# Kernel tuning notes

Measured on AMD Instinct MI355X. Metric: run time of the kernel, lower is better.

The kernel has to match this reference:

```python
import jax, jax.numpy as jnp
import numpy as np


def _lstm_step(x, h, c, Wih, Whh, bih, bhh):
    # PyTorch LSTMCell gate order: i, f, g, o
    g = x @ Wih.T + bih + h @ Whh.T + bhh
    i, f, gg, o = jnp.split(g, 4, axis=1)
    c = jax.nn.sigmoid(f) * c + jax.nn.sigmoid(i) * jnp.tanh(gg)
    h = jax.nn.sigmoid(o) * jnp.tanh(c)
    return h, c


def _canvas2seq(canvas):
    # Valid objects (row-sum >= 0) compacted to the front, rest padded with -1.
    mask = canvas.sum(axis=2) >= 0                       # [B, 25]
    order = jnp.argsort(jnp.where(mask, 0, 1), axis=1, stable=True)
    gathered = jnp.take_along_axis(canvas, order[:, :, None], axis=1)
    smask = jnp.take_along_axis(mask, order, axis=1)
    return jnp.where(smask[:, :, None], gathered, jnp.float32(-1.0))


def _canvas_encode(canvas, Wobj, bobj, ce_Wih, ce_Whh, ce_bih, ce_bhh):
    seq = _canvas2seq(canvas)                            # [B, 25, 4]
    x = seq @ Wobj.T + bobj                              # [B, 25, 64]
    B = x.shape[0]
    h = jnp.zeros((B, 64), x.dtype)
    c = jnp.zeros((B, 64), x.dtype)

    def step(carry, xt):
        h, c = carry
        h, c = _lstm_step(xt, h, c, ce_Wih, ce_Whh, ce_bih, ce_bhh)
        return (h, c), None

    (h, _), _ = jax.lax.scan(step, (h, c), jnp.swapaxes(x, 0, 1))
    return h


def setup_inputs() -> dict:
    key = jax.random.key(0)
    ks = jax.random.split(key, 16)
    B, T, V = 256, 65, 10000
    IN, H = 64, 128
    s = 0.05
    inp = {}
    inp["inst"] = jax.random.randint(ks[0], (B, T), 0, V)
    inp["prev_canvas"] = jax.random.uniform(ks[1], (B, 25, 4), dtype=jnp.float32)
    inp["final_canvas"] = jax.random.uniform(ks[2], (B, 25, 4), dtype=jnp.float32)
    inp["target_obj"] = jax.random.normal(ks[3], (B, 4), dtype=jnp.float32)
    inp["embed_W"] = jax.random.normal(ks[4], (V + 1, IN), dtype=jnp.float32) * s
    inp["Wih"] = jax.random.normal(ks[5], (4 * H, IN), dtype=jnp.float32) * s
    inp["Whh"] = jax.random.normal(ks[6], (4 * H, H), dtype=jnp.float32) * s
    inp["bih"] = jnp.zeros((4 * H,), jnp.float32)
    inp["bhh"] = jnp.zeros((4 * H,), jnp.float32)
    inp["Wout"] = jax.random.normal(ks[7], (V + 1, H), dtype=jnp.float32) * s
    inp["bout"] = jnp.zeros((V + 1,), jnp.float32)
    inp["Wtgt"] = jax.random.normal(ks[8], (IN, 4), dtype=jnp.float32) * s
    inp["btgt"] = jnp.zeros((IN,), jnp.float32)
    inp["Wobj"] = jax.random.normal(ks[9], (64, 4), dtype=jnp.float32) * s
    inp["bobj"] = jnp.zeros((64,), jnp.float32)
    inp["ce_Wih"] = jax.random.normal(ks[10], (256, 64), dtype=jnp.float32) * s
    inp["ce_Whh"] = jax.random.normal(ks[11], (256, 64), dtype=jnp.float32) * s
    inp["ce_bih"] = jnp.zeros((256,), jnp.float32)
    inp["ce_bhh"] = jnp.zeros((256,), jnp.float32)
    return inp


def reference(inst, prev_canvas, final_canvas, target_obj,
              embed_W, Wih, Whh, bih, bhh, Wout, bout,
              Wtgt, btgt, Wobj, bobj, ce_Wih, ce_Whh, ce_bih, ce_bhh):
    B, H = inst.shape[0], 128
    tgt_emb = target_obj @ Wtgt.T + btgt                 # [B, 64]
    enc = (_canvas_encode(prev_canvas, Wobj, bobj, ce_Wih, ce_Whh, ce_bih, ce_bhh)
           + _canvas_encode(final_canvas, Wobj, bobj, ce_Wih, ce_Whh, ce_bih, ce_bhh))
    h = jnp.zeros((B, H), jnp.float32)
    c = jnp.zeros((B, H), jnp.float32)
    h, c = _lstm_step(enc, h, c, Wih, Whh, bih, bhh)
    h, c = _lstm_step(tgt_emb, h, c, Wih, Whh, bih, bhh)

    tokens = inst[:, :-1].T                              # [T-1, B]

    def step(carry, it):
        h, c = carry
        xt = embed_W[it]                                 # [B, 64]
        h, c = _lstm_step(xt, h, c, Wih, Whh, bih, bhh)
        lp = jax.nn.log_softmax(h @ Wout.T + bout, axis=1)
        return (h, c), lp

    _, lps = jax.lax.scan(step, (h, c), tokens)          # [T-1, B, V+1]
    return jnp.swapaxes(lps, 0, 1)                       # [B, T-1, V+1]
```

## Files before the change

kernel.cpp:

```cpp
#include <hip/hip_runtime.h>
#include <stdint.h>

typedef __attribute__((ext_vector_type(4))) float f32x4;
typedef __attribute__((ext_vector_type(8))) short s16x8;
typedef __attribute__((ext_vector_type(8))) unsigned short us8;

__device__ __forceinline__ float bf2f(unsigned short u){
  union { unsigned int i; float f; } v; v.i = ((unsigned int)u) << 16; return v.f;
}
__device__ __forceinline__ unsigned short f2bf(float f){
  union { float f; unsigned int i; } v; v.f = f;
  unsigned int r = v.i + 0x7FFFu + ((v.i >> 16) & 1u);
  return (unsigned short)(r >> 16);
}
__device__ __forceinline__ float sigm(float x){ return 1.0f / (1.0f + __expf(-x)); }

#define NA (10240*128)
#define NB 10240
#define ND 512
#define NE (256*64)
#define NF 32768

__global__ void k_prep(const float* __restrict__ Wout, const float* __restrict__ bout,
                       const float* __restrict__ bih,  const float* __restrict__ bhh,
                       const float* __restrict__ tobj, const float* __restrict__ Wtgt,
                       const float* __restrict__ btgt,
                       const float* __restrict__ ceWih, const float* __restrict__ ceWhh,
                       unsigned short* __restrict__ WoutP, float* __restrict__ boutP,
                       float* __restrict__ bsum, float* __restrict__ tgt,
                       unsigned short* __restrict__ cePack)
{
  int tid = blockIdx.x * 256 + threadIdx.x;
  if (tid < NA){
    int vv = tid >> 7, k = tid & 127;
    float val = (vv < 10001) ? Wout[vv*128 + k] : 0.0f;
    WoutP[tid] = f2bf(val);
  } else if (tid < NA+NB){
    int vv = tid - NA;
    boutP[vv] = (vv < 10001) ? bout[vv] : -1e30f;
  } else if (tid < NA+NB+ND){
    int g = tid - NA - NB;
    bsum[g] = bih[g] + bhh[g];
  } else if (tid < NA+NB+ND+NE){
    int i = tid - NA - NB - ND; int b = i >> 6, j = i & 63;
    const float* to = tobj + b*4; const float* wt = Wtgt + j*4;
    tgt[i] = btgt[j] + to[0]*wt[0] + to[1]*wt[1] + to[2]*wt[2] + to[3]*wt[3];
  } else if (tid < NA+NB+ND+NE+NF){
    int i = tid - NA - NB - ND - NE;
    int half = i >> 14;
    int r = (i >> 6) & 255;
    int k = i & 63;
    int k8 = k >> 3;
    int slot = ((k8 ^ (r & 7)) << 3) | (k & 7);
    const float* src = half ? ceWhh : ceWih;
    cePack[half*16384 + r*64 + slot] = f2bf(src[r*64 + k]);
  }
}

__global__ __launch_bounds__(256) void k_canvas(
    const float* __restrict__ prevC, const float* __restrict__ finC,
    const float* __restrict__ Wobj,  const float* __restrict__ bobj,
    const unsigned short* __restrict__ cePack,
    const float* __restrict__ cebih, const float* __restrict__ cebhh,
    float* __restrict__ encP, float* __restrict__ encF)
{
  __shared__ unsigned short wih[256*64] __attribute__((aligned(16)));
  __shared__ unsigned short whh[256*64] __attribute__((aligned(16)));
  __shared__ float seq[25*4];
  __shared__ float xb[64] __attribute__((aligned(16)));
  __shared__ float hb[2][64] __attribute__((aligned(16)));
  __shared__ float gates[256];
  __shared__ float wobj_s[256];
  __shared__ float bobj_s[64];
  __shared__ float bsum_ce[256];

  int tid = threadIdx.x;
  int b = blockIdx.x & 255;
  int which = blockIdx.x >> 8;
  const float* canvas = (which ? finC : prevC) + b*100;

  {
    const us8* cp = (const us8*)cePack;
    us8* wl = (us8*)wih;
    us8* hl = (us8*)whh;
    for (int i = tid; i < 2048; i += 256){
      wl[i] = cp[i];
      hl[i] = cp[2048 + i];
    }
  }
  wobj_s[tid] = Wobj[tid];
  if (tid < 64) bobj_s[tid] = bobj[tid];
  bsum_ce[tid] = cebih[tid] + cebhh[tid];
  if (tid < 64) hb[0][tid] = 0.0f;
  if (tid == 0){
    int pos = 0;
    for (int i = 0; i < 25; i++){
      float a0=canvas[i*4+0], a1=canvas[i*4+1], a2=canvas[i*4+2], a3=canvas[i*4+3];
      if (a0+a1+a2+a3 >= 0.0f){
        seq[pos*4+0]=a0; seq[pos*4+1]=a1; seq[pos*4+2]=a2; seq[pos*4+3]=a3; pos++;
      }
    }
    for (; pos < 25; pos++){
      seq[pos*4+0]=-1.0f; seq[pos*4+1]=-1.0f; seq[pos*4+2]=-1.0f; seq[pos*4+3]=-1.0f;
    }
  }
  __syncthreads();

  float creg = 0.0f;
  int cur = 0;
  const float4* x4 = (const float4*)xb;

  for (int t = 0; t < 25; t++){
    if (tid < 64){
      float a = bobj_s[tid];
      a += wobj_s[tid*4+0]*seq[t*4+0] + wobj_s[tid*4+1]*seq[t*4+1]
         + wobj_s[tid*4+2]*seq[t*4+2] + wobj_s[tid*4+3]*seq[t*4+3];
      xb[tid] = a;
    }
    __syncthreads();
    float acc = bsum_ce[tid];
    const float4* h4 = (const float4*)hb[cur];
    int rowoff = tid*64;
    int sw = tid & 7;
    #pragma unroll
    for (int k8 = 0; k8 < 8; k8++){
      int slot = ((k8 ^ sw) * 8);
      us8 w1 = *reinterpret_cast<const us8*>(&wih[rowoff + slot]);
      us8 w2 = *reinterpret_cast<const us8*>(&whh[rowoff + slot]);
      float4 xa = x4[2*k8], xc = x4[2*k8+1];
      float4 ha = h4[2*k8], hc = h4[2*k8+1];
      acc += bf2f(w1[0])*xa.x + bf2f(w1[1])*xa.y + bf2f(w1[2])*xa.z + bf2f(w1[3])*xa.w;
      acc += bf2f(w1[4])*xc.x + bf2f(w1[5])*xc.y + bf2f(w1[6])*xc.z + bf2f(w1[7])*xc.w;
      acc += bf2f(w2[0])*ha.x + bf2f(w2[1])*ha.y + bf2f(w2[2])*ha.z + bf2f(w2[3])*ha.w;
      acc += bf2f(w2[4])*hc.x + bf2f(w2[5])*hc.y + bf2f(w2[6])*hc.z + bf2f(w2[7])*hc.w;
    }
    gates[tid] = acc;
    __syncthreads();
    if (tid < 64){
      float i_ = sigm(gates[tid]);
      float f_ = sigm(gates[64+tid]);
      float g_ = tanhf(gates[128+tid]);
      float o_ = sigm(gates[192+tid]);
      creg = f_*creg + i_*g_;
      hb[cur^1][tid] = o_ * tanhf(creg);
    }
    __syncthreads();
    cur ^= 1;
  }
  if (tid < 64){
    (which ? encF : encP)[b*64 + tid] = hb[cur][tid];
  }
}

__global__ __launch_bounds__(512, 2) void k_rec(
    const float* __restrict__ Whh, const float* __restrict__ Wih,
    const float* __restrict__ bsum, const int* __restrict__ inst,
    const float* __restrict__ embW, const float* __restrict__ tgt,
    const float* __restrict__ encP, const float* __restrict__ encF,
    unsigned short* __restrict__ Hout)
{
  int b = blockIdx.x;
  int g = threadIdx.x;
  __shared__ float xb[2][64] __attribute__((aligned(16)));
  __shared__ float hb[2][128] __attribute__((aligned(16)));
  __shared__ float gates[512];

  float wreg[128];
  float ureg[64];
  {
    const float4* wrow = (const float4*)(Whh + g*128);
    #pragma unroll
    for (int k4 = 0; k4 < 32; k4++){
      float4 w = wrow[k4];
      wreg[4*k4+0]=w.x; wreg[4*k4+1]=w.y; wreg[4*k4+2]=w.z; wreg[4*k4+3]=w.w;
    }
    const float4* urow = (const float4*)(Wih + g*64);
    #pragma unroll
    for (int k4 = 0; k4 < 16; k4++){
      float4 w = urow[k4];
      ureg[4*k4+0]=w.x; ureg[4*k4+1]=w.y; ureg[4*k4+2]=w.z; ureg[4*k4+3]=w.w;
    }
  }
  float bz = bsum[g];
  float creg = 0.0f;
  if (g < 128) hb[0][g] = 0.0f;
  if (g < 64)  xb[0][g] = encP[b*64+g] + encF[b*64+g];
  int cur = 0;
  __syncthreads();

  for (int s = 0; s < 66; s++){
    float a0 = bz, a1 = 0.0f, a2 = 0.0f, a3 = 0.0f;
    const float4* h4 = (const float4*)hb[cur];
    const float4* x4 = (const float4*)xb[cur];
    #pragma unroll
    for (int k4 = 0; k4 < 32; k4 += 4){
      float4 h0 = h4[k4], h1 = h4[k4+1], h2 = h4[k4+2], h3 = h4[k4+3];
      a0 += wreg[4*k4+0]*h0.x + wreg[4*k4+1]*h0.y + wreg[4*k4+2]*h0.z + wreg[4*k4+3]*h0.w;
      a1 += wreg[4*k4+4]*h1.x + wreg[4*k4+5]*h1.y + wreg[4*k4+6]*h1.z + wreg[4*k4+7]*h1.w;
      a2 += wreg[4*k4+8]*h2.x + wreg[4*k4+9]*h2.y + wreg[4*k4+10]*h2.z + wreg[4*k4+11]*h2.w;
      a3 += wreg[4*k4+12]*h3.x + wreg[4*k4+13]*h3.y + wreg[4*k4+14]*h3.z + wreg[4*k4+15]*h3.w;
    }
    #pragma unroll
    for (int k4 = 0; k4 < 16; k4 += 4){
      float4 x0 = x4[k4], x1 = x4[k4+1], x2 = x4[k4+2], x3 = x4[k4+3];
      a0 += ureg[4*k4+0]*x0.x + ureg[4*k4+1]*x0.y + ureg[4*k4+2]*x0.z + ureg[4*k4+3]*x0.w;
      a1 += ureg[4*k4+4]*x1.x + ureg[4*k4+5]*x1.y + ureg[4*k4+6]*x1.z + ureg[4*k4+7]*x1.w;
      a2 += ureg[4*k4+8]*x2.x + ureg[4*k4+9]*x2.y + ureg[4*k4+10]*x2.z + ureg[4*k4+11]*x2.w;
      a3 += ureg[4*k4+12]*x3.x + ureg[4*k4+13]*x3.y + ureg[4*k4+14]*x3.z + ureg[4*k4+15]*x3.w;
    }
    gates[g] = (a0 + a1) + (a2 + a3);
    __syncthreads();
    if (g < 128){
      float i_ = sigm(gates[g]);
      float f_ = sigm(gates[128+g]);
      float g_ = tanhf(gates[256+g]);
      float o_ = sigm(gates[384+g]);
      creg = f_*creg + i_*g_;
      float h = o_ * tanhf(creg);
      hb[cur^1][g] = h;
      if (s >= 2) Hout[((size_t)(b*64 + (s-2)))*128 + g] = f2bf(h);
    } else if (g < 192 && s < 65){
      int l = g - 128;
      float v;
      if (s + 1 == 1) v = tgt[b*64 + l];
      else { int tok = inst[b*65 + (s - 1)]; v = embW[tok*64 + l]; }
      xb[cur^1][l] = v;
    }
    __syncthreads();
    cur ^= 1;
  }
}

__global__ __launch_bounds__(512, 2) void k_out(
    const unsigned short* __restrict__ Hout, const unsigned short* __restrict__ WoutP,
    const float* __restrict__ boutP, float* __restrict__ out)
{
  extern __shared__ float stage[];
  __shared__ float rs_l[8][64];
  __shared__ float lse_l[64];

  int blk = blockIdx.x;
  int r0 = blk * 64;
  int tid = threadIdx.x;
  int w = tid >> 6;
  int l = tid & 63;
  int lm = l & 15;
  int lq = l >> 4;
  int kof = lq * 8;
  size_t obase = (size_t)r0 * 10001u;

  s16x8 af[4][4];
  #pragma unroll
  for (int c = 0; c < 4; c++){
    const s16x8* ap = (const s16x8*)(Hout + (size_t)(r0 + c*16 + lm)*128 + kof);
    #pragma unroll
    for (int kk = 0; kk < 4; kk++) af[c][kk] = ap[kk*4];
  }

  s16x8 b0[4], b1[4], b2[4];
#define LOADB(dst, tl) { \
    const s16x8* bp_ = (const s16x8*)(WoutP + (size_t)((tl)*16 + lm)*128 + kof); \
    dst[0] = bp_[0]; dst[1] = bp_[4]; dst[2] = bp_[8]; dst[3] = bp_[12]; }

  float rs[4][4] = {};
#define P1C(buf, tl) { \
    f32x4 a0_ = {0,0,0,0}, a1_ = {0,0,0,0}, a2_ = {0,0,0,0}, a3_ = {0,0,0,0}; \
    _Pragma("unroll") \
    for (int kk = 0; kk < 4; kk++){ \
      a0_ = __builtin_amdgcn_mfma_f32_16x16x32_bf16(af[0][kk], buf[kk], a0_, 0, 0, 0); \
      a1_ = __builtin_amdgcn_mfma_f32_16x16x32_bf16(af[1][kk], buf[kk], a1_, 0, 0, 0); \
      a2_ = __builtin_amdgcn_mfma_f32_16x16x32_bf16(af[2][kk], buf[kk], a2_, 0, 0, 0); \
      a3_ = __builtin_amdgcn_mfma_f32_16x16x32_bf16(af[3][kk], buf[kk], a3_, 0, 0, 0); } \
    float bo_ = boutP[(tl)*16 + lm]; \
    _Pragma("unroll") \
    for (int i = 0; i < 4; i++){ \
      rs[0][i] += __expf(a0_[i] + bo_); rs[1][i] += __expf(a1_[i] + bo_); \
      rs[2][i] += __expf(a2_[i] + bo_); rs[3][i] += __expf(a3_[i] + bo_); } }

  {
    int tl = w;
    LOADB(b0, tl); LOADB(b1, tl + 8);
    for (int p = 0; p < 26; p++){
      LOADB(b2, tl + 16); P1C(b0, tl);
      LOADB(b0, tl + 24); P1C(b1, tl + 8);
      LOADB(b1, tl + 32); P1C(b2, tl + 16);
      tl += 24;
    }
    P1C(b0, tl);
    P1C(b1, tl + 8);
  }

  #pragma unroll
  for (int c = 0; c < 4; c++){
    #pragma unroll
    for (int i = 0; i < 4; i++){
      float s = rs[c][i];
      s += __shfl_xor(s, 1); s += __shfl_xor(s, 2);
      s += __shfl_xor(s, 4); s += __shfl_xor(s, 8);
      rs[c][i] = s;
    }
  }
  if (lm == 0){
    #pragma unroll
    for (int c = 0; c < 4; c++)
      #pragma unroll
      for (int i = 0; i < 4; i++)
        rs_l[w][c*16 + lq*4 + i] = rs[c][i];
  }

#define T2(c,q) ((c)*32 + w*4 + (q))
  LOADB(b0, T2(0,0)); LOADB(b1, T2(0,1));

#define BAR() { asm volatile("s_waitcnt lgkmcnt(0)" ::: "memory"); __builtin_amdgcn_s_barrier(); }

  BAR();
  if (tid < 64){
    float s = rs_l[0][tid] + rs_l[1][tid] + rs_l[2][tid] + rs_l[3][tid]
            + rs_l[4][tid] + rs_l[5][tid] + rs_l[6][tid] + rs_l[7][tid];
    lse_l[tid] = logf(s);
  }
  BAR();
  float ml[4][4];
  #pragma unroll
  for (int c = 0; c < 4; c++)
    #pragma unroll
    for (int i = 0; i < 4; i++)
      ml[c][i] = lse_l[c*16 + lq*4 + i];

#define P2C(buf, tl, q) { \
    f32x4 a0_ = {0,0,0,0}, a1_ = {0,0,0,0}, a2_ = {0,0,0,0}, a3_ = {0,0,0,0}; \
    _Pragma("unroll") \
    for (int kk = 0; kk < 4; kk++){ \
      a0_ = __builtin_amdgcn_mfma_f32_16x16x32_bf16(af[0][kk], buf[kk], a0_, 0, 0, 0); \
      a1_ = __builtin_amdgcn_mfma_f32_16x16x32_bf16(af[1][kk], buf[kk], a1_, 0, 0, 0); \
      a2_ = __builtin_amdgcn_mfma_f32_16x16x32_bf16(af[2][kk], buf[kk], a2_, 0, 0, 0); \
      a3_ = __builtin_amdgcn_mfma_f32_16x16x32_bf16(af[3][kk], buf[kk], a3_, 0, 0, 0); } \
    float bo_ = boutP[(tl)*16 + lm]; \
    int colq_ = (w*4 + (q))*16 + lm; \
    _Pragma("unroll") \
    for (int i = 0; i < 4; i++){ \
      stage[(0*16 + lq*4 + i)*520 + colq_] = a0_[i] + bo_ - ml[0][i]; \
      stage[(1*16 + lq*4 + i)*520 + colq_] = a1_[i] + bo_ - ml[1][i]; \
      stage[(2*16 + lq*4 + i)*520 + colq_] = a2_[i] + bo_ - ml[2][i]; \
      stage[(3*16 + lq*4 + i)*520 + colq_] = a3_[i] + bo_ - ml[3][i]; } }

#define WPHASE(c) { \
    int vbase_ = (c)*512; \
    if ((c) < 19){ \
      _Pragma("unroll 4") \
      for (int j = 0; j < 64; j++){ \
        __builtin_nontemporal_store(stage[j*520 + tid], \
            &out[obase + (size_t)j*10001u + (unsigned)(vbase_ + tid)]); } \
    } else { \
      if (tid < 273){ \
        _Pragma("unroll 4") \
        for (int j = 0; j < 64; j++){ \
          __builtin_nontemporal_store(stage[j*520 + tid], \
              &out[obase + (size_t)j*10001u + (unsigned)(vbase_ + tid)]); } } } }

#define CHUNK(ba,bb,bc,c) { \
    LOADB(bc, T2(c,2));   P2C(ba, T2(c,0), 0); \
    LOADB(ba, T2(c,3));   P2C(bb, T2(c,1), 1); \
    LOADB(bb, T2((c)+1,0)); P2C(bc, T2(c,2), 2); \
    LOADB(bc, T2((c)+1,1)); P2C(ba, T2(c,3), 3); \
    BAR(); WPHASE(c); BAR(); }

  for (int cb = 0; cb < 18; cb += 3){
    CHUNK(b0, b1, b2, cb);
    CHUNK(b1, b2, b0, cb + 1);
    CHUNK(b2, b0, b1, cb + 2);
  }
  CHUNK(b0, b1, b2, 18);
  LOADB(b0, T2(19,2)); P2C(b1, T2(19,0), 0);
  LOADB(b1, T2(19,3)); P2C(b2, T2(19,1), 1);
  P2C(b0, T2(19,2), 2);
  P2C(b1, T2(19,3), 3);
  BAR();
  WPHASE(19);
}

extern "C" void kernel_launch(void* const* d_in, const int* in_sizes, int n_in,
                              void* d_out, int out_size, void* d_ws, size_t ws_size,
                              hipStream_t stream)
{
  (void)in_sizes; (void)n_in; (void)out_size; (void)ws_size;
  const int*   inst    = (const int*)  d_in[0];
  const float* prevC   = (const float*)d_in[1];
  const float* finC    = (const float*)d_in[2];
  const float* tobj    = (const float*)d_in[3];
  const float* embW    = (const float*)d_in[4];
  const float* Wih     = (const float*)d_in[5];
  const float* Whh     = (const float*)d_in[6];
  const float* bih     = (const float*)d_in[7];
  const float* bhh     = (const float*)d_in[8];
  const float* Wout    = (const float*)d_in[9];
  const float* bout    = (const float*)d_in[10];
  const float* Wtgt    = (const float*)d_in[11];
  const float* btgt    = (const float*)d_in[12];
  const float* Wobj    = (const float*)d_in[13];
  const float* bobj    = (const float*)d_in[14];
  const float* ceWih   = (const float*)d_in[15];
  const float* ceWhh   = (const float*)d_in[16];
  const float* cebih   = (const float*)d_in[17];
  const float* cebhh   = (const float*)d_in[18];

  char* ws = (char*)d_ws;
  unsigned short* WoutP = (unsigned short*)(ws + 0);
  float* boutP = (float*)(ws + 2621440);
  float* bsum  = (float*)(ws + 2662400);
  float* tgt   = (float*)(ws + 2664448);
  float* encP  = (float*)(ws + 2729984);
  float* encF  = (float*)(ws + 2795520);
  unsigned short* Hout = (unsigned short*)(ws + 2861056);
  unsigned short* cePack = (unsigned short*)(ws + 7055360);
  float* out = (float*)d_out;

  hipFuncSetAttribute((const void*)k_out,
                      hipFuncAttributeMaxDynamicSharedMemorySize, 133120);

  k_prep  <<<5354, 256, 0, stream>>>(Wout, bout, bih, bhh, tobj, Wtgt, btgt,
                                     ceWih, ceWhh, WoutP, boutP, bsum, tgt, cePack);
  k_canvas<<<512, 256, 0, stream>>>(prevC, finC, Wobj, bobj, cePack,
                                    cebih, cebhh, encP, encF);
  k_rec   <<<256, 512, 0, stream>>>(Whh, Wih, bsum, inst, embW, tgt, encP, encF, Hout);
  k_out   <<<256, 512, 133120, stream>>>(Hout, WoutP, boutP, out);
}
```

Before: 529.5 us.

## Split output projection into logsumexp kernel and high-occupancy write kernel

The fused output kernel, which computed the row logsumexp and then recomputed and wrote the log-probabilities with a large 130KB shared staging buffer, is split in two. The first kernel computes the logsumexp per row into a global workspace buffer. A second kernel works on 16-row tiles across 1024 blocks with a small 16KB stage, aiming for higher occupancy and more parallelism in the write-bandwidth-bound phase. The cost is an extra launch and reloading Wout for each of the 4x more row blocks.

```diff
diff --git a/kernel.cpp b/kernel.cpp
--- a/kernel.cpp
+++ b/kernel.cpp
@@ -231,13 +231,11 @@
   }
 }
 
-__global__ __launch_bounds__(512, 2) void k_out(
+__global__ __launch_bounds__(512, 2) void k_lse(
     const unsigned short* __restrict__ Hout, const unsigned short* __restrict__ WoutP,
-    const float* __restrict__ boutP, float* __restrict__ out)
-{
-  extern __shared__ float stage[];
+    const float* __restrict__ boutP, float* __restrict__ lseG)
+{
   __shared__ float rs_l[8][64];
-  __shared__ float lse_l[64];
 
   int blk = blockIdx.x;
   int r0 = blk * 64;
@@ -247,7 +245,6 @@
   int lm = l & 15;
   int lq = l >> 4;
   int kof = lq * 8;
-  size_t obase = (size_t)r0 * 10001u;
 
   s16x8 af[4][4];
   #pragma unroll
@@ -258,12 +255,12 @@
   }
 
   s16x8 b0[4], b1[4], b2[4];
-#define LOADB(dst, tl) { \
+#define L_LOADB(dst, tl) { \
     const s16x8* bp_ = (const s16x8*)(WoutP + (size_t)((tl)*16 + lm)*128 + kof); \
     dst[0] = bp_[0]; dst[1] = bp_[4]; dst[2] = bp_[8]; dst[3] = bp_[12]; }
 
   float rs[4][4] = {};
-#define P1C(buf, tl) { \
+#define L_P1C(buf, tl) { \
     f32x4 a0_ = {0,0,0,0}, a1_ = {0,0,0,0}, a2_ = {0,0,0,0}, a3_ = {0,0,0,0}; \
     _Pragma("unroll") \
     for (int kk = 0; kk < 4; kk++){ \
@@ -279,15 +276,15 @@
 
   {
     int tl = w;
-    LOADB(b0, tl); LOADB(b1, tl + 8);
+    L_LOADB(b0, tl); L_LOADB(b1, tl + 8);
     for (int p = 0; p < 26; p++){
-      LOADB(b2, tl + 16); P1C(b0, tl);
-      LOADB(b0, tl + 24); P1C(b1, tl + 8);
-      LOADB(b1, tl + 32); P1C(b2, tl + 16);
+      L_LOADB(b2, tl + 16); L_P1C(b0, tl);
+      L_LOADB(b0, tl + 24); L_P1C(b1, tl + 8);
+      L_LOADB(b1, tl + 32); L_P1C(b2, tl + 16);
       tl += 24;
     }
-    P1C(b0, tl);
-    P1C(b1, tl + 8);
+    L_P1C(b0, tl);
+    L_P1C(b1, tl + 8);
   }
 
   #pragma unroll
@@ -307,76 +304,90 @@
       for (int i = 0; i < 4; i++)
         rs_l[w][c*16 + lq*4 + i] = rs[c][i];
   }
-
-#define T2(c,q) ((c)*32 + w*4 + (q))
-  LOADB(b0, T2(0,0)); LOADB(b1, T2(0,1));
-
-#define BAR() { asm volatile("s_waitcnt lgkmcnt(0)" ::: "memory"); __builtin_amdgcn_s_barrier(); }
-
-  BAR();
+  __syncthreads();
   if (tid < 64){
     float s = rs_l[0][tid] + rs_l[1][tid] + rs_l[2][tid] + rs_l[3][tid]
             + rs_l[4][tid] + rs_l[5][tid] + rs_l[6][tid] + rs_l[7][tid];
-    lse_l[tid] = logf(s);
-  }
-  BAR();
-  float ml[4][4];
+    lseG[r0 + tid] = logf(s);
+  }
+}
+
+__global__ __launch_bounds__(512, 8) void k_write(
+    const unsigned short* __restrict__ Hout, const unsigned short* __restrict__ WoutP,
+    const float* __restrict__ boutP, const float* __restrict__ lseG,
+    float* __restrict__ out)
+{
+  __shared__ float stage[16*260];
+
+  int blk = blockIdx.x;
+  int r0 = blk * 16;
+  int tid = threadIdx.x;
+  int w = tid >> 6;
+  int l = tid & 63;
+  int lm = l & 15;
+  int lq = l >> 4;
+  int kof = lq * 8;
+  size_t obase = (size_t)r0 * 10001u;
+
+  s16x8 af[4];
+  {
+    const s16x8* ap = (const s16x8*)(Hout + (size_t)(r0 + lm)*128 + kof);
+    #pragma unroll
+    for (int kk = 0; kk < 4; kk++) af[kk] = ap[kk*4];
+  }
+  float ml[4];
   #pragma unroll
-  for (int c = 0; c < 4; c++)
-    #pragma unroll
-    for (int i = 0; i < 4; i++)
-      ml[c][i] = lse_l[c*16 + lq*4 + i];
-
-#define P2C(buf, tl, q) { \
-    f32x4 a0_ = {0,0,0,0}, a1_ = {0,0,0,0}, a2_ = {0,0,0,0}, a3_ = {0,0,0,0}; \
+  for (int i = 0; i < 4; i++) ml[i] = lseG[r0 + lq*4 + i];
+
+  s16x8 b0[4], b1[4], b2[4], b3[4];
+#define W_LOADB(dst, tl) { \
+    const s16x8* bp_ = (const s16x8*)(WoutP + (size_t)((tl)*16 + lm)*128 + kof); \
+    dst[0] = bp_[0]; dst[1] = bp_[4]; dst[2] = bp_[8]; dst[3] = bp_[12]; }
+
+#define W_P2C(buf, tl, q) { \
+    f32x4 a_ = {0,0,0,0}; \
     _Pragma("unroll") \
-    for (int kk = 0; kk < 4; kk++){ \
-      a0_ = __builtin_amdgcn_mfma_f32_16x16x32_bf16(af[0][kk], buf[kk], a0_, 0, 0, 0); \
-      a1_ = __builtin_amdgcn_mfma_f32_16x16x32_bf16(af[1][kk], buf[kk], a1_, 0, 0, 0); \
-      a2_ = __builtin_amdgcn_mfma_f32_16x16x32_bf16(af[2][kk], buf[kk], a2_, 0, 0, 0); \
-      a3_ = __builtin_amdgcn_mfma_f32_16x16x32_bf16(af[3][kk], buf[kk], a3_, 0, 0, 0); } \
+    for (int kk = 0; kk < 4; kk++) \
+      a_ = __builtin_amdgcn_mfma_f32_16x16x32_bf16(af[kk], buf[kk], a_, 0, 0, 0); \
     float bo_ = boutP[(tl)*16 + lm]; \
-    int colq_ = (w*4 + (q))*16 + lm; \
+    int colq_ = (w*2 + (q))*16 + lm; \
     _Pragma("unroll") \
-    for (int i = 0; i < 4; i++){ \
-      stage[(0*16 + lq*4 + i)*520 + colq_] = a0_[i] + bo_ - ml[0][i]; \
-      stage[(1*16 + lq*4 + i)*520 + colq_] = a1_[i] + bo_ - ml[1][i]; \
-      stage[(2*16 + lq*4 + i)*520 + colq_] = a2_[i] + bo_ - ml[2][i]; \
-      stage[(3*16 + lq*4 + i)*520 + colq_] = a3_[i] + bo_ - ml[3][i]; } }
-
-#define WPHASE(c) { \
-    int vbase_ = (c)*512; \
-    if ((c) < 19){ \
-      _Pragma("unroll 4") \
-      for (int j = 0; j < 64; j++){ \
-        __builtin_nontemporal_store(stage[j*520 + tid], \
-            &out[obase + (size_t)j*10001u + (unsigned)(vbase_ + tid)]); } \
+    for (int i = 0; i < 4; i++) \
+      stage[(lq*4 + i)*260 + colq_] = a_[i] + bo_ - ml[i]; }
+
+#define W_BAR() { asm volatile("s_waitcnt lgkmcnt(0)" ::: "memory"); __builtin_amdgcn_s_barrier(); }
+
+#define W_WPH(c) { \
+    int vbase_ = (c)*256; \
+    if ((c) < 39){ \
+      _Pragma("unroll") \
+      for (int j = 0; j < 8; j++){ \
+        int e_ = j*512 + tid; int row_ = e_ >> 8; int cc_ = e_ & 255; \
+        __builtin_nontemporal_store(stage[row_*260 + cc_], \
+            &out[obase + (size_t)row_*10001u + (unsigned)(vbase_ + cc_)]); } \
     } else { \
-      if (tid < 273){ \
-        _Pragma("unroll 4") \
-        for (int j = 0; j < 64; j++){ \
-          __builtin_nontemporal_store(stage[j*520 + tid], \
-              &out[obase + (size_t)j*10001u + (unsigned)(vbase_ + tid)]); } } } }
-
-#define CHUNK(ba,bb,bc,c) { \
-    LOADB(bc, T2(c,2));   P2C(ba, T2(c,0), 0); \
-    LOADB(ba, T2(c,3));   P2C(bb, T2(c,1), 1); \
-    LOADB(bb, T2((c)+1,0)); P2C(bc, T2(c,2), 2); \
-    LOADB(bc, T2((c)+1,1)); P2C(ba, T2(c,3), 3); \
-    BAR(); WPHASE(c); BAR(); }
-
-  for (int cb = 0; cb < 18; cb += 3){
-    CHUNK(b0, b1, b2, cb);
-    CHUNK(b1, b2, b0, cb + 1);
-    CHUNK(b2, b0, b1, cb + 2);
-  }
-  CHUNK(b0, b1, b2, 18);
-  LOADB(b0, T2(19,2)); P2C(b1, T2(19,0), 0);
-  LOADB(b1, T2(19,3)); P2C(b2, T2(19,1), 1);
-  P2C(b0, T2(19,2), 2);
-  P2C(b1, T2(19,3), 3);
-  BAR();
-  WPHASE(19);
+      _Pragma("unroll") \
+      for (int j = 0; j < 8; j++){ \
+        int e_ = j*512 + tid; int row_ = e_ >> 8; int cc_ = e_ & 255; \
+        if (vbase_ + cc_ < 10001) \
+          __builtin_nontemporal_store(stage[row_*260 + cc_], \
+              &out[obase + (size_t)row_*10001u + (unsigned)(vbase_ + cc_)]); } } }
+
+#define W_CHUNK(curA, curB, nxtA, nxtB, c) { \
+    if ((c) + 1 < 40){ \
+      W_LOADB(nxtA, ((c)+1)*16 + w*2); \
+      W_LOADB(nxtB, ((c)+1)*16 + w*2 + 1); } \
+    W_P2C(curA, (c)*16 + w*2, 0); \
+    W_P2C(curB, (c)*16 + w*2 + 1, 1); \
+    W_BAR(); \
+    W_WPH(c); \
+    W_BAR(); }
+
+  W_LOADB(b0, w*2); W_LOADB(b1, w*2 + 1);
+  for (int c = 0; c < 40; c += 2){
+    W_CHUNK(b0, b1, b2, b3, c);
+    W_CHUNK(b2, b3, b0, b1, c + 1);
+  }
 }
 
 extern "C" void kernel_launch(void* const* d_in, const int* in_sizes, int n_in,
@@ -413,15 +424,14 @@
   float* encF  = (float*)(ws + 2795520);
   unsigned short* Hout = (unsigned short*)(ws + 2861056);
   unsigned short* cePack = (unsigned short*)(ws + 7055360);
+  float* lseG  = (float*)(ws + 7120896);
   float* out = (float*)d_out;
-
-  hipFuncSetAttribute((const void*)k_out,
-                      hipFuncAttributeMaxDynamicSharedMemorySize, 133120);
 
   k_prep  <<<5354, 256, 0, stream>>>(Wout, bout, bih, bhh, tobj, Wtgt, btgt,
                                      ceWih, ceWhh, WoutP, boutP, bsum, tgt, cePack);
   k_canvas<<<512, 256, 0, stream>>>(prevC, finC, Wobj, bobj, cePack,
                                     cebih, cebhh, encP, encF);
   k_rec   <<<256, 512, 0, stream>>>(Whh, Wih, bsum, inst, embW, tgt, encP, encF, Hout);
-  k_out   <<<256, 512, 133120, stream>>>(Hout, WoutP, boutP, out);
-}
+  k_lse   <<<256, 512, 0, stream>>>(Hout, WoutP, boutP, lseG);
+  k_write <<<1024, 512, 0, stream>>>(Hout, WoutP, boutP, lseG, out);
+}
```

New measurement: 1.194 ms. 2.26x slower.

## Store logits directly from MFMA registers, drop LDS staging in output kernel

Applied to the files above, without the earlier changes.

The output projection kernel no longer stages each 512-column chunk through 130KB of shared memory with barriers before nontemporal coalesced stores. Each wave now writes its MFMA results straight to global memory, 16 contiguous floats per row segment, and the B-operand pipeline goes from triple to double buffering. Launch bounds rise to 4 blocks per SM. This removes the LDS round trip and the barrier stalls, but global stores become narrower, scattered 64-byte segments per row and are no longer nontemporal, which may hurt write coalescing on this write-bound kernel.

```diff
diff --git a/kernel.cpp b/kernel.cpp
--- a/kernel.cpp
+++ b/kernel.cpp
@@ -231,11 +231,10 @@
   }
 }
 
-__global__ __launch_bounds__(512, 2) void k_out(
+__global__ __launch_bounds__(512, 4) void k_out(
     const unsigned short* __restrict__ Hout, const unsigned short* __restrict__ WoutP,
     const float* __restrict__ boutP, float* __restrict__ out)
 {
-  extern __shared__ float stage[];
   __shared__ float rs_l[8][64];
   __shared__ float lse_l[64];
 
@@ -247,7 +246,6 @@
   int lm = l & 15;
   int lq = l >> 4;
   int kof = lq * 8;
-  size_t obase = (size_t)r0 * 10001u;
 
   s16x8 af[4][4];
   #pragma unroll
@@ -257,7 +255,7 @@
     for (int kk = 0; kk < 4; kk++) af[c][kk] = ap[kk*4];
   }
 
-  s16x8 b0[4], b1[4], b2[4];
+  s16x8 b0[4], b1[4];
 #define LOADB(dst, tl) { \
     const s16x8* bp_ = (const s16x8*)(WoutP + (size_t)((tl)*16 + lm)*128 + kof); \
     dst[0] = bp_[0]; dst[1] = bp_[4]; dst[2] = bp_[8]; dst[3] = bp_[12]; }
@@ -279,14 +277,14 @@
 
   {
     int tl = w;
-    LOADB(b0, tl); LOADB(b1, tl + 8);
-    for (int p = 0; p < 26; p++){
-      LOADB(b2, tl + 16); P1C(b0, tl);
-      LOADB(b0, tl + 24); P1C(b1, tl + 8);
-      LOADB(b1, tl + 32); P1C(b2, tl + 16);
-      tl += 24;
+    LOADB(b0, tl);
+    for (int p = 0; p < 39; p++){
+      LOADB(b1, tl + 8);  P1C(b0, tl);
+      LOADB(b0, tl + 16); P1C(b1, tl + 8);
+      tl += 16;
     }
     P1C(b0, tl);
+    LOADB(b1, tl + 8);
     P1C(b1, tl + 8);
   }
 
@@ -307,19 +305,13 @@
       for (int i = 0; i < 4; i++)
         rs_l[w][c*16 + lq*4 + i] = rs[c][i];
   }
-
-#define T2(c,q) ((c)*32 + w*4 + (q))
-  LOADB(b0, T2(0,0)); LOADB(b1, T2(0,1));
-
-#define BAR() { asm volatile("s_waitcnt lgkmcnt(0)" ::: "memory"); __builtin_amdgcn_s_barrier(); }
-
-  BAR();
+  __syncthreads();
   if (tid < 64){
     float s = rs_l[0][tid] + rs_l[1][tid] + rs_l[2][tid] + rs_l[3][tid]
             + rs_l[4][tid] + rs_l[5][tid] + rs_l[6][tid] + rs_l[7][tid];
     lse_l[tid] = logf(s);
   }
-  BAR();
+  __syncthreads();
   float ml[4][4];
   #pragma unroll
   for (int c = 0; c < 4; c++)
@@ -327,7 +319,12 @@
     for (int i = 0; i < 4; i++)
       ml[c][i] = lse_l[c*16 + lq*4 + i];
 
-#define P2C(buf, tl, q) { \
+  float* ob = out + (size_t)r0 * 10001u;
+  unsigned vb[4];
+  #pragma unroll
+  for (int i = 0; i < 4; i++) vb[i] = (unsigned)((lq*4 + i)*10001 + lm);
+
+#define ST(buf, t) { \
     f32x4 a0_ = {0,0,0,0}, a1_ = {0,0,0,0}, a2_ = {0,0,0,0}, a3_ = {0,0,0,0}; \
     _Pragma("unroll") \
     for (int kk = 0; kk < 4; kk++){ \
@@ -335,48 +332,33 @@
       a1_ = __builtin_amdgcn_mfma_f32_16x16x32_bf16(af[1][kk], buf[kk], a1_, 0, 0, 0); \
       a2_ = __builtin_amdgcn_mfma_f32_16x16x32_bf16(af[2][kk], buf[kk], a2_, 0, 0, 0); \
       a3_ = __builtin_amdgcn_mfma_f32_16x16x32_bf16(af[3][kk], buf[kk], a3_, 0, 0, 0); } \
-    float bo_ = boutP[(tl)*16 + lm]; \
-    int colq_ = (w*4 + (q))*16 + lm; \
-    _Pragma("unroll") \
-    for (int i = 0; i < 4; i++){ \
-      stage[(0*16 + lq*4 + i)*520 + colq_] = a0_[i] + bo_ - ml[0][i]; \
-      stage[(1*16 + lq*4 + i)*520 + colq_] = a1_[i] + bo_ - ml[1][i]; \
-      stage[(2*16 + lq*4 + i)*520 + colq_] = a2_[i] + bo_ - ml[2][i]; \
-      stage[(3*16 + lq*4 + i)*520 + colq_] = a3_[i] + bo_ - ml[3][i]; } }
-
-#define WPHASE(c) { \
-    int vbase_ = (c)*512; \
-    if ((c) < 19){ \
-      _Pragma("unroll 4") \
-      for (int j = 0; j < 64; j++){ \
-        __builtin_nontemporal_store(stage[j*520 + tid], \
-            &out[obase + (size_t)j*10001u + (unsigned)(vbase_ + tid)]); } \
-    } else { \
-      if (tid < 273){ \
-        _Pragma("unroll 4") \
-        for (int j = 0; j < 64; j++){ \
-          __builtin_nontemporal_store(stage[j*520 + tid], \
-              &out[obase + (size_t)j*10001u + (unsigned)(vbase_ + tid)]); } } } }
-
-#define CHUNK(ba,bb,bc,c) { \
-    LOADB(bc, T2(c,2));   P2C(ba, T2(c,0), 0); \
-    LOADB(ba, T2(c,3));   P2C(bb, T2(c,1), 1); \
-    LOADB(bb, T2((c)+1,0)); P2C(bc, T2(c,2), 2); \
-    LOADB(bc, T2((c)+1,1)); P2C(ba, T2(c,3), 3); \
-    BAR(); WPHASE(c); BAR(); }
-
-  for (int cb = 0; cb < 18; cb += 3){
-    CHUNK(b0, b1, b2, cb);
-    CHUNK(b1, b2, b0, cb + 1);
-    CHUNK(b2, b0, b1, cb + 2);
-  }
-  CHUNK(b0, b1, b2, 18);
-  LOADB(b0, T2(19,2)); P2C(b1, T2(19,0), 0);
-  LOADB(b1, T2(19,3)); P2C(b2, T2(19,1), 1);
-  P2C(b0, T2(19,2), 2);
-  P2C(b1, T2(19,3), 3);
-  BAR();
-  WPHASE(19);
+    float bo_ = boutP[(t)*16 + lm]; \
+    float* op_ = ob + (size_t)(t)*16; \
+    if ((t) < 625){ \
+      _Pragma("unroll") \
+      for (int i = 0; i < 4; i++){ \
+        op_[vb[i]]              = a0_[i] + bo_ - ml[0][i]; \
+        op_[vb[i] + 1u*160016u] = a1_[i] + bo_ - ml[1][i]; \
+        op_[vb[i] + 2u*160016u] = a2_[i] + bo_ - ml[2][i]; \
+        op_[vb[i] + 3u*160016u] = a3_[i] + bo_ - ml[3][i]; } \
+    } else if ((t) == 625 && lm == 0){ \
+      _Pragma("unroll") \
+      for (int i = 0; i < 4; i++){ \
+        op_[vb[i]]              = a0_[i] + bo_ - ml[0][i]; \
+        op_[vb[i] + 1u*160016u] = a1_[i] + bo_ - ml[1][i]; \
+        op_[vb[i] + 2u*160016u] = a2_[i] + bo_ - ml[2][i]; \
+        op_[vb[i] + 3u*160016u] = a3_[i] + bo_ - ml[3][i]; } } }
+
+  {
+    int t = w;
+    LOADB(b0, t);
+    for (int p = 0; p < 39; p++){
+      LOADB(b1, t + 8);  ST(b0, t);
+      LOADB(b0, t + 16); ST(b1, t + 8);
+      t += 16;
+    }
+    ST(b0, t);
+  }
 }
 
 extern "C" void kernel_launch(void* const* d_in, const int* in_sizes, int n_in,
@@ -415,13 +397,10 @@
   unsigned short* cePack = (unsigned short*)(ws + 7055360);
   float* out = (float*)d_out;
 
-  hipFuncSetAttribute((const void*)k_out,
-                      hipFuncAttributeMaxDynamicSharedMemorySize, 133120);
-
   k_prep  <<<5354, 256, 0, stream>>>(Wout, bout, bih, bhh, tobj, Wtgt, btgt,
                                      ceWih, ceWhh, WoutP, boutP, bsum, tgt, cePack);
   k_canvas<<<512, 256, 0, stream>>>(prevC, finC, Wobj, bobj, cePack,
                                     cebih, cebhh, encP, encF);
   k_rec   <<<256, 512, 0, stream>>>(Whh, Wih, bsum, inst, embW, tgt, encP, encF, Hout);
-  k_out   <<<256, 512, 133120, stream>>>(Hout, WoutP, boutP, out);
-}
+  k_out   <<<256, 512, 0, stream>>>(Hout, WoutP, boutP, out);
+}
```

Measured after the change: 758.3 us. +43.2%, slower.

## Halve k_out row tile to 32 rows to double blocks and occupancy

Applied to the files above, without the earlier changes.

The output projection/log-softmax kernel now processes 32 rows per block instead of 64. It launches 512 blocks with half the staging shared memory and asks for 4 blocks per CU in its launch bounds. The aim is more resident waves to hide memory latency and to spread the large output write across more CUs. In exchange, each Wout tile loaded from memory is reused across only half as many rows, so weight traffic roughly doubles.

```diff
diff --git a/kernel.cpp b/kernel.cpp
--- a/kernel.cpp
+++ b/kernel.cpp
@@ -231,16 +231,16 @@
   }
 }
 
-__global__ __launch_bounds__(512, 2) void k_out(
+__global__ __launch_bounds__(512, 4) void k_out(
     const unsigned short* __restrict__ Hout, const unsigned short* __restrict__ WoutP,
     const float* __restrict__ boutP, float* __restrict__ out)
 {
   extern __shared__ float stage[];
-  __shared__ float rs_l[8][64];
-  __shared__ float lse_l[64];
+  __shared__ float rs_l[8][32];
+  __shared__ float lse_l[32];
 
   int blk = blockIdx.x;
-  int r0 = blk * 64;
+  int r0 = blk * 32;
   int tid = threadIdx.x;
   int w = tid >> 6;
   int l = tid & 63;
@@ -249,9 +249,9 @@
   int kof = lq * 8;
   size_t obase = (size_t)r0 * 10001u;
 
-  s16x8 af[4][4];
+  s16x8 af[2][4];
   #pragma unroll
-  for (int c = 0; c < 4; c++){
+  for (int c = 0; c < 2; c++){
     const s16x8* ap = (const s16x8*)(Hout + (size_t)(r0 + c*16 + lm)*128 + kof);
     #pragma unroll
     for (int kk = 0; kk < 4; kk++) af[c][kk] = ap[kk*4];
@@ -262,20 +262,16 @@
     const s16x8* bp_ = (const s16x8*)(WoutP + (size_t)((tl)*16 + lm)*128 + kof); \
     dst[0] = bp_[0]; dst[1] = bp_[4]; dst[2] = bp_[8]; dst[3] = bp_[12]; }
 
-  float rs[4][4] = {};
+  float rs[2][4] = {};
 #define P1C(buf, tl) { \
-    f32x4 a0_ = {0,0,0,0}, a1_ = {0,0,0,0}, a2_ = {0,0,0,0}, a3_ = {0,0,0,0}; \
+    f32x4 a0_ = {0,0,0,0}, a1_ = {0,0,0,0}; \
     _Pragma("unroll") \
     for (int kk = 0; kk < 4; kk++){ \
       a0_ = __builtin_amdgcn_mfma_f32_16x16x32_bf16(af[0][kk], buf[kk], a0_, 0, 0, 0); \
-      a1_ = __builtin_amdgcn_mfma_f32_16x16x32_bf16(af[1][kk], buf[kk], a1_, 0, 0, 0); \
-      a2_ = __builtin_amdgcn_mfma_f32_16x16x32_bf16(af[2][kk], buf[kk], a2_, 0, 0, 0); \
-      a3_ = __builtin_amdgcn_mfma_f32_16x16x32_bf16(af[3][kk], buf[kk], a3_, 0, 0, 0); } \
+      a1_ = __builtin_amdgcn_mfma_f32_16x16x32_bf16(af[1][kk], buf[kk], a1_, 0, 0, 0); } \
     float bo_ = boutP[(tl)*16 + lm]; \
     _Pragma("unroll") \
-    for (int i = 0; i < 4; i++){ \
-      rs[0][i] += __expf(a0_[i] + bo_); rs[1][i] += __expf(a1_[i] + bo_); \
-      rs[2][i] += __expf(a2_[i] + bo_); rs[3][i] += __expf(a3_[i] + bo_); } }
+    for (int i = 0; i < 4; i++){ rs[0][i] += __expf(a0_[i] + bo_); rs[1][i] += __expf(a1_[i] + bo_); } }
 
   {
     int tl = w;
@@ -291,7 +287,7 @@
   }
 
   #pragma unroll
-  for (int c = 0; c < 4; c++){
+  for (int c = 0; c < 2; c++){
     #pragma unroll
     for (int i = 0; i < 4; i++){
       float s = rs[c][i];
@@ -302,7 +298,7 @@
   }
   if (lm == 0){
     #pragma unroll
-    for (int c = 0; c < 4; c++)
+    for (int c = 0; c < 2; c++)
       #pragma unroll
       for (int i = 0; i < 4; i++)
         rs_l[w][c*16 + lq*4 + i] = rs[c][i];
@@ -314,53 +310,51 @@
 #define BAR() { asm volatile("s_waitcnt lgkmcnt(0)" ::: "memory"); __builtin_amdgcn_s_barrier(); }
 
   BAR();
-  if (tid < 64){
+  if (tid < 32){
     float s = rs_l[0][tid] + rs_l[1][tid] + rs_l[2][tid] + rs_l[3][tid]
             + rs_l[4][tid] + rs_l[5][tid] + rs_l[6][tid] + rs_l[7][tid];
     lse_l[tid] = logf(s);
   }
   BAR();
-  float ml[4][4];
+  float ml[2][4];
   #pragma unroll
-  for (int c = 0; c < 4; c++)
+  for (int c = 0; c < 2; c++)
     #pragma unroll
     for (int i = 0; i < 4; i++)
       ml[c][i] = lse_l[c*16 + lq*4 + i];
 
 #define P2C(buf, tl, q) { \
-    f32x4 a0_ = {0,0,0,0}, a1_ = {0,0,0,0}, a2_ = {0,0,0,0}, a3_ = {0,0,0,0}; \
+    f32x4 a0_ = {0,0,0,0}, a1_ = {0,0,0,0}; \
     _Pragma("unroll") \
     for (int kk = 0; kk < 4; kk++){ \
       a0_ = __builtin_amdgcn_mfma_f32_16x16x32_bf16(af[0][kk], buf[kk], a0_, 0, 0, 0); \
-      a1_ = __builtin_amdgcn_mfma_f32_16x16x32_bf16(af[1][kk], buf[kk], a1_, 0, 0, 0); \
-      a2_ = __builtin_amdgcn_mfma_f32_16x16x32_bf16(af[2][kk], buf[kk], a2_, 0, 0, 0); \
-      a3_ = __builtin_amdgcn_mfma_f32_16x16x32_bf16(af[3][kk], buf[kk], a3_, 0, 0, 0); } \
+      a1_ = __builtin_amdgcn_mfma_f32_16x16x32_bf16(af[1][kk], buf[kk], a1_, 0, 0, 0); } \
     float bo_ = boutP[(tl)*16 + lm]; \
     int colq_ = (w*4 + (q))*16 + lm; \
     _Pragma("unroll") \
     for (int i = 0; i < 4; i++){ \
-      stage[(0*16 + lq*4 + i)*520 + colq_] = a0_[i] + bo_ - ml[0][i]; \
-      stage[(1*16 + lq*4 + i)*520 + colq_] = a1_[i] + bo_ - ml[1][i]; \
-      stage[(2*16 + lq*4 + i)*520 + colq_] = a2_[i] + bo_ - ml[2][i]; \
-      stage[(3*16 + lq*4 + i)*520 + colq_] = a3_[i] + bo_ - ml[3][i]; } }
+      stage[(0*16 + lq*4 + i)*516 + colq_] = a0_[i] + bo_ - ml[0][i]; \
+      stage[(1*16 + lq*4 + i)*516 + colq_] = a1_[i] + bo_ - ml[1][i]; } }
 
 #define WPHASE(c) { \
     int vbase_ = (c)*512; \
     if ((c) < 19){ \
       _Pragma("unroll 4") \
-      for (int j = 0; j < 64; j++){ \
-        __builtin_nontemporal_store(stage[j*520 + tid], \
-            &out[obase + (size_t)j*10001u + (unsigned)(vbase_ + tid)]); } \
+      for (int j = 0; j < 32; j++){ \
+        int e_ = j*512 + tid; int row_ = e_ >> 9; int cc_ = e_ & 511; \
+        __builtin_nontemporal_store(stage[row_*516 + cc_], \
+            &out[obase + (size_t)row_*10001u + (unsigned)(vbase_ + cc_)]); } \
     } else { \
-      if (tid < 273){ \
-        _Pragma("unroll 4") \
-        for (int j = 0; j < 64; j++){ \
-          __builtin_nontemporal_store(stage[j*520 + tid], \
-              &out[obase + (size_t)j*10001u + (unsigned)(vbase_ + tid)]); } } } }
+      _Pragma("unroll 4") \
+      for (int j = 0; j < 32; j++){ \
+        int e_ = j*512 + tid; int row_ = e_ >> 9; int cc_ = e_ & 511; \
+        if (vbase_ + cc_ < 10001) \
+          __builtin_nontemporal_store(stage[row_*516 + cc_], \
+              &out[obase + (size_t)row_*10001u + (unsigned)(vbase_ + cc_)]); } } }
 
 #define CHUNK(ba,bb,bc,c) { \
-    LOADB(bc, T2(c,2));   P2C(ba, T2(c,0), 0); \
-    LOADB(ba, T2(c,3));   P2C(bb, T2(c,1), 1); \
+    LOADB(bc, T2(c,2));     P2C(ba, T2(c,0), 0); \
+    LOADB(ba, T2(c,3));     P2C(bb, T2(c,1), 1); \
     LOADB(bb, T2((c)+1,0)); P2C(bc, T2(c,2), 2); \
     LOADB(bc, T2((c)+1,1)); P2C(ba, T2(c,3), 3); \
     BAR(); WPHASE(c); BAR(); }
@@ -416,12 +410,12 @@
   float* out = (float*)d_out;
 
   hipFuncSetAttribute((const void*)k_out,
-                      hipFuncAttributeMaxDynamicSharedMemorySize, 133120);
+                      hipFuncAttributeMaxDynamicSharedMemorySize, 66048);
 
   k_prep  <<<5354, 256, 0, stream>>>(Wout, bout, bih, bhh, tobj, Wtgt, btgt,
                                      ceWih, ceWhh, WoutP, boutP, bsum, tgt, cePack);
   k_canvas<<<512, 256, 0, stream>>>(prevC, finC, Wobj, bobj, cePack,
                                     cebih, cebhh, encP, encF);
   k_rec   <<<256, 512, 0, stream>>>(Whh, Wih, bsum, inst, embW, tgt, encP, encF, Hout);
-  k_out   <<<256, 512, 133120, stream>>>(Hout, WoutP, boutP, out);
-}
+  k_out   <<<512, 512, 66048, stream>>>(Hout, WoutP, boutP, out);
+}
```

After: 561.6 us. +6.1%, slower.
